# Kernel tuning notes

Hardware: AMD Instinct MI355X
Metric: run time of the kernel (lower is better)

The kernel has to match this reference:

```python
import jax, jax.numpy as jnp
import numpy as np


def _forward(x, wc, we, Wb1, bb1, Wb2, bb2, Wr1, br1, Wr2, br2,
             Wq1, bq1, Wq2, bq2, Wq3, bq3, Wo1, bo1, Wo2, bo2, Wo3, bo3, scale):
    bs, c, h, w = x.shape
    Hs, Ws = scale * h, scale * w
    fh = (jnp.arange(Hs, dtype=jnp.float32) + 0.5) / scale
    fw = (jnp.arange(Ws, dtype=jnp.float32) + 0.5) / scale
    coor_h = fh - jnp.floor(fh + 0.001) - 0.5  # [Hs] fractional phase
    coor_w = fw - jnp.floor(fw + 0.001) - 0.5  # [Ws]
    ones_hw = jnp.ones((Hs, Ws), jnp.float32)
    meta = jnp.stack([ones_hw, ones_hw / scale,
                      jnp.broadcast_to(coor_h[:, None], (Hs, Ws)),
                      jnp.broadcast_to(coor_w[None, :], (Hs, Ws))], 0)  # [4,Hs,Ws]
    chan_mean = x.mean(axis=(0, 2, 3))  # [c]
    chan_scale = jnp.concatenate([chan_mean[:, None], jnp.ones((c, 3), jnp.float32)], axis=1)  # [c,4]
    inp = meta[None] * chan_scale[:, :, None, None]  # [c,4,Hs,Ws]

    # body: 1x1x1 Conv3d over spectral-channel axis c
    lin = lambda W, b, t: jnp.einsum('oc,cfhw->ofhw', W, t) + b[:, None, None, None]
    emb = jax.nn.relu(lin(Wb2, bb2, jax.nn.relu(lin(Wb1, bb1, inp))))  # [c,4,Hs,Ws]

    # offset head: Conv2d 1x1 with batch = c, features = 4 -> 2
    lin2 = lambda W, b, t: jnp.einsum('of,cfhw->cohw', W, t) + b[None, :, None, None]
    off = lin2(Wo3, bo3, jax.nn.relu(lin2(Wo2, bo2, jax.nn.relu(lin2(Wo1, bo1, emb)))))  # [c,2,Hs,Ws]

    # routing_1: Conv3d over c -> 1 channel, sigmoid
    r = jax.nn.sigmoid(lin(Wr2, br2, jax.nn.relu(lin(Wr1, br1, emb))))[0]  # [4,Hs,Ws]
    # routing_2: Conv2d 1x1 over the 4 meta-features -> E experts
    lin3 = lambda W, b, t: jnp.einsum('of,fhw->ohw', W, t) + b[:, None, None]
    rw = jax.nn.sigmoid(lin3(Wq3, bq3, jax.nn.relu(lin3(Wq2, bq2, jax.nn.relu(lin3(Wq1, bq1, r))))))  # [E,Hs,Ws]

    # per-channel offset grid_sample (bilinear, zeros padding, align_corners=True)
    px0 = fw - 0.5  # [Ws] base source x coord
    py0 = fh - 0.5  # [Hs]

    def sample(img, offx, offy):  # img [bs,h,w]; off* [Hs,Ws]
        px = px0[None, :] + offx
        py = py0[:, None] + offy
        x0 = jnp.floor(px); y0 = jnp.floor(py)
        wx = px - x0; wy = py - y0
        x0i = x0.astype(jnp.int32); y0i = y0.astype(jnp.int32)
        def g(yi, xi):
            v = ((xi >= 0) & (xi <= w - 1) & (yi >= 0) & (yi <= h - 1)).astype(img.dtype)
            return img[:, jnp.clip(yi, 0, h - 1), jnp.clip(xi, 0, w - 1)] * v[None]
        return (g(y0i, x0i) * ((1 - wy) * (1 - wx))[None]
                + g(y0i, x0i + 1) * ((1 - wy) * wx)[None]
                + g(y0i + 1, x0i) * (wy * (1 - wx))[None]
                + g(y0i + 1, x0i + 1) * (wy * wx)[None])

    fea0 = jax.vmap(lambda xi, oi: sample(xi, oi[0], oi[1]),
                    in_axes=(1, 0), out_axes=1)(x, off)  # [bs,c,Hs,Ws]

    # per-pixel expert-mixed compress/expand: (sum_e r_e Wc_e) f then (sum_e r_e We_e)
    mid = jnp.einsum('ehw,ekc,bchw->bkhw', rw, wc, fea0)   # [bs,c//8,Hs,Ws]
    out = jnp.einsum('ehw,eck,bkhw->bchw', rw, we, mid)    # [bs,c,Hs,Ws]
    return out + fea0


def setup_inputs() -> dict:
    key = jax.random.key(0)
    ks = jax.random.split(key, 32)
    bs, c, h, w = 4, 64, 64, 64
    E, k = 4, c // 8
    s = 0.05
    d = {
        'x': jax.random.normal(ks[0], (bs, c, h, w), jnp.float32),
        'wc': jax.random.normal(ks[1], (E, k, c), jnp.float32) * s,
        'we': jax.random.normal(ks[2], (E, c, k), jnp.float32) * s,
        'Wb1': jax.random.normal(ks[3], (c, c), jnp.float32) * s,
        'bb1': jax.random.normal(ks[4], (c,), jnp.float32) * s,
        'Wb2': jax.random.normal(ks[5], (c, c), jnp.float32) * s,
        'bb2': jax.random.normal(ks[6], (c,), jnp.float32) * s,
        'Wr1': jax.random.normal(ks[7], (64, c), jnp.float32) * s,
        'br1': jax.random.normal(ks[8], (64,), jnp.float32) * s,
        'Wr2': jax.random.normal(ks[9], (1, 64), jnp.float32) * s,
        'br2': jax.random.normal(ks[10], (1,), jnp.float32) * s,
        'Wq1': jax.random.normal(ks[11], (64, 4), jnp.float32) * s,
        'bq1': jax.random.normal(ks[12], (64,), jnp.float32) * s,
        'Wq2': jax.random.normal(ks[13], (64, 64), jnp.float32) * s,
        'bq2': jax.random.normal(ks[14], (64,), jnp.float32) * s,
        'Wq3': jax.random.normal(ks[15], (E, 64), jnp.float32) * s,
        'bq3': jax.random.normal(ks[16], (E,), jnp.float32) * s,
        'Wo1': jax.random.normal(ks[17], (64, 4), jnp.float32) * s,
        'bo1': jax.random.normal(ks[18], (64,), jnp.float32) * s,
        'Wo2': jax.random.normal(ks[19], (64, 64), jnp.float32) * s,
        'bo2': jax.random.normal(ks[20], (64,), jnp.float32) * s,
        'Wo3': jax.random.normal(ks[21], (2, 64), jnp.float32) * s,
        'bo3': jax.random.normal(ks[22], (2,), jnp.float32) * s,
        'scale': 4,
    }
    return d


def reference(x, wc, we, Wb1, bb1, Wb2, bb2, Wr1, br1, Wr2, br2,
              Wq1, bq1, Wq2, bq2, Wq3, bq3, Wo1, bo1, Wo2, bo2, Wo3, bo3, scale):
    return _forward(x, wc, we, Wb1, bb1, Wb2, bb2, Wr1, br1, Wr2, br2,
                    Wq1, bq1, Wq2, bq2, Wq3, bq3, Wo1, bo1, Wo2, bo2, Wo3, bo3, int(scale))
```

## Files before the change

### kernel.cpp

```cpp
#include <hip/hip_runtime.h>


__device__ __forceinline__ float relu_(float v){ return fmaxf(v, 0.f); }
__device__ __forceinline__ float sigm_(float v){ return 1.f/(1.f + __expf(-v)); }

__global__ void k_mean(const float* __restrict__ x, float* __restrict__ ws) {
  const int ch = blockIdx.x, b = blockIdx.y, t = threadIdx.x;
  const float* xp = x + (size_t)(b*64 + ch)*4096;
  const float4* p4 = reinterpret_cast<const float4*>(xp);
  float4 v0 = p4[t], v1 = p4[t+256], v2 = p4[t+512], v3 = p4[t+768];
  float s = ((v0.x+v0.y)+(v0.z+v0.w)) + ((v1.x+v1.y)+(v1.z+v1.w))
          + ((v2.x+v2.y)+(v2.z+v2.w)) + ((v3.x+v3.y)+(v3.z+v3.w));
  __shared__ float red[256];
  red[t] = s; __syncthreads();
  for (int off = 128; off > 0; off >>= 1) {
    if (t < off) red[t] += red[t + off];
    __syncthreads();
  }
  if (t == 0) ws[b*64 + ch] = red[0];

  float* dst = ws + 21760 + (size_t)(b*64 + ch)*4752;
  if (t < 66) {
    float4* drow = reinterpret_cast<float4*>(dst + t*72);
    const float4 z = make_float4(0.f, 0.f, 0.f, 0.f);
    if (t == 0 || t == 65) {
      #pragma unroll
      for (int q = 0; q < 18; ++q) drow[q] = z;
    } else {
      const float4* srow = reinterpret_cast<const float4*>(xp + (t-1)*64);
      drow[0] = z;
      #pragma unroll
      for (int q = 0; q < 16; ++q) drow[1+q] = srow[q];
      drow[17] = z;
    }
  }
}

__launch_bounds__(256)
__global__ void k_phase(const float* __restrict__ wc, const float* __restrict__ we,
    const float* __restrict__ Wb1, const float* __restrict__ bb1,
    const float* __restrict__ Wb2, const float* __restrict__ bb2,
    const float* __restrict__ Wr1, const float* __restrict__ br1,
    const float* __restrict__ Wr2, const float* __restrict__ br2,
    const float* __restrict__ Wq1, const float* __restrict__ bq1,
    const float* __restrict__ Wq2, const float* __restrict__ bq2,
    const float* __restrict__ Wq3, const float* __restrict__ bq3,
    const float* __restrict__ Wo1, const float* __restrict__ bo1,
    const float* __restrict__ Wo2, const float* __restrict__ bo2,
    const float* __restrict__ Wo3, const float* __restrict__ bo3,
    float* __restrict__ ws)
{
  const int p = blockIdx.x, pi = p >> 2, pj = p & 3;
  const int t = threadIdx.x;
  const float chv = 0.25f*pi - 0.375f, cwv = 0.25f*pj - 0.375f;

  __shared__ float WbL1[64*66];
  __shared__ float WbL2[64*66];
  __shared__ float WrL1[64*66];
  __shared__ float WqL2[64*66];
  __shared__ __align__(16) float Wo2L[4096];
  __shared__ __align__(16) float Wo1L[256];
  __shared__ __align__(16) float wcL[2048];
  __shared__ __align__(16) float weL[2048];
  __shared__ float Wo3L[128];
  __shared__ float Wq1L[256], Wq3L[256];
  __shared__ float Wr2L[64];
  __shared__ float bb1L[64], bb2L[64], br1L[64], bq1L[64], bq2L[64];
  __shared__ float bo1L[64], bo2L[64];

  __shared__ float meanL[64];
  __shared__ __align__(16) float t1L[64][4];
  __shared__ __align__(16) float embL[64][4];
  __shared__ __align__(16) float rpL[64][4];
  __shared__ float r4[4];
  __shared__ float q1L[64], q2L[64];
  __shared__ float rwL[4];
  __shared__ float oxL[64][4], oyL[64][4];
  __shared__ float oxF[64], oyF[64];

  {
    const float* srcs[4] = {Wb1, Wb2, Wr1, Wq2};
    float* dsts[4] = {WbL1, WbL2, WrL1, WqL2};
    for (int m = 0; m < 4; ++m) {
      const float4* W4 = reinterpret_cast<const float4*>(srcs[m]);
      float* WL = dsts[m];
      for (int v = t; v < 1024; v += 256) {
        float4 d = W4[v];
        const int r = v >> 4, c = (v & 15) << 2;
        float* q = &WL[r*66 + c];
        q[0] = d.x; q[1] = d.y; q[2] = d.z; q[3] = d.w;
      }
    }
    for (int v = t; v < 1024; v += 256)
      reinterpret_cast<float4*>(Wo2L)[v] = reinterpret_cast<const float4*>(Wo2)[v];
    for (int v = t; v < 512; v += 256) {
      reinterpret_cast<float4*>(wcL)[v] = reinterpret_cast<const float4*>(wc)[v];
      reinterpret_cast<float4*>(weL)[v] = reinterpret_cast<const float4*>(we)[v];
    }
    if (t < 64) {
      reinterpret_cast<float4*>(Wo1L)[t] = reinterpret_cast<const float4*>(Wo1)[t];
      reinterpret_cast<float4*>(Wq1L)[t] = reinterpret_cast<const float4*>(Wq1)[t];
      reinterpret_cast<float4*>(Wq3L)[t] = reinterpret_cast<const float4*>(Wq3)[t];
      bb1L[t] = bb1[t]; bb2L[t] = bb2[t]; br1L[t] = br1[t];
      bq1L[t] = bq1[t]; bq2L[t] = bq2[t];
      bo1L[t] = bo1[t]; bo2L[t] = bo2[t];
      Wr2L[t] = Wr2[t];
      const float* wsp = ws;
      meanL[t] = (wsp[t] + wsp[64+t] + wsp[128+t] + wsp[192+t]) * (1.f/16384.f);
    }
    if (t >= 64 && t < 192) Wo3L[t-64] = Wo3[t-64];
  }
  __syncthreads();

  if (t < 64) {
    float a0 = 0.f, as = 0.f;
    const float* row = &WbL1[t*66];
    #pragma unroll 8
    for (int c = 0; c < 64; ++c) { float w = row[c]; a0 += w*meanL[c]; as += w; }
    float bb = bb1L[t];
    t1L[t][0] = relu_(a0 + bb);
    t1L[t][1] = relu_(0.25f*as + bb);
    t1L[t][2] = relu_(chv*as + bb);
    t1L[t][3] = relu_(cwv*as + bb);
  }
  __syncthreads();
  if (t < 64) {
    float bb = bb2L[t];
    float e0=bb,e1=bb,e2=bb,e3=bb;
    const float* row = &WbL2[t*66];
    #pragma unroll 8
    for (int c = 0; c < 64; ++c) {
      float w = row[c];
      float4 tv = *reinterpret_cast<const float4*>(&t1L[c][0]);
      e0 += w*tv.x; e1 += w*tv.y; e2 += w*tv.z; e3 += w*tv.w;
    }
    embL[t][0]=relu_(e0); embL[t][1]=relu_(e1); embL[t][2]=relu_(e2); embL[t][3]=relu_(e3);
  }
  __syncthreads();
  if (t < 64) {
    float bb = br1L[t];
    float p0=bb,p1=bb,p2=bb,p3=bb;
    const float* row = &WrL1[t*66];
    #pragma unroll 8
    for (int c = 0; c < 64; ++c) {
      float w = row[c];
      float4 ev = *reinterpret_cast<const float4*>(&embL[c][0]);
      p0 += w*ev.x; p1 += w*ev.y; p2 += w*ev.z; p3 += w*ev.w;
    }
    rpL[t][0]=relu_(p0); rpL[t][1]=relu_(p1); rpL[t][2]=relu_(p2); rpL[t][3]=relu_(p3);
  }
  __syncthreads();
  if (t < 4) {
    float acc = br2[0];
    #pragma unroll 8
    for (int c = 0; c < 64; ++c) acc += Wr2L[c]*rpL[c][t];
    r4[t] = sigm_(acc);
  }
  __syncthreads();
  if (t < 64) {
    float acc = bq1L[t];
    #pragma unroll
    for (int f = 0; f < 4; ++f) acc += Wq1L[t*4+f]*r4[f];
    q1L[t] = relu_(acc);
  }
  __syncthreads();
  if (t < 64) {
    float acc = bq2L[t];
    const float* row = &WqL2[t*66];
    #pragma unroll 8
    for (int c = 0; c < 64; ++c) acc += row[c]*q1L[c];
    q2L[t] = relu_(acc);
  }
  __syncthreads();
  if (t < 4) {
    float acc = bq3[t];
    #pragma unroll 8
    for (int c = 0; c < 64; ++c) acc += Wq3L[t*64+c]*q2L[c];
    rwL[t] = sigm_(acc);
  }
  __syncthreads();

  {
    const int ch = t & 63, q = t >> 6;
    const float4 e = *reinterpret_cast<const float4*>(&embL[ch][0]);
    float v1[64];
    #pragma unroll
    for (int o = 0; o < 64; ++o) {
      float4 w = *reinterpret_cast<const float4*>(&Wo1L[o*4]);
      v1[o] = relu_(w.x*e.x + w.y*e.y + w.z*e.z + w.w*e.w + bo1L[o]);
    }
    float ox = 0.f, oy = 0.f;
    for (int o = q*16; o < q*16+16; ++o) {
      float acc = bo2L[o];
      const float4* row = reinterpret_cast<const float4*>(&Wo2L[o*64]);
      #pragma unroll
      for (int k = 0; k < 16; ++k) {
        float4 w = row[k];
        acc += w.x*v1[4*k+0] + w.y*v1[4*k+1] + w.z*v1[4*k+2] + w.w*v1[4*k+3];
      }
      acc = relu_(acc);
      ox += Wo3L[o]*acc;
      oy += Wo3L[64+o]*acc;
    }
    oxL[ch][q] = ox; oyL[ch][q] = oy;
  }
  __syncthreads();
  if (t < 64) {
    oxF[t] = oxL[t][0]+oxL[t][1]+oxL[t][2]+oxL[t][3] + bo3[0];
    oyF[t] = oyL[t][0]+oyL[t][1]+oyL[t][2]+oyL[t][3] + bo3[1];
  }
  __syncthreads();

  {
    const float r0 = rwL[0], r1 = rwL[1], r2 = rwL[2], r3 = rwL[3];
    for (int idx = t; idx < 1024; idx += 256) {
      const int ch = idx >> 4, k = idx & 15;
      float v;
      if (k < 8) {
        v = r0*wcL[(0*8+k)*64+ch] + r1*wcL[(1*8+k)*64+ch]
          + r2*wcL[(2*8+k)*64+ch] + r3*wcL[(3*8+k)*64+ch];
      } else {
        const int kk = k - 8;
        v = r0*weL[(0*64+ch)*8+kk] + r1*weL[(1*64+ch)*8+kk]
          + r2*weL[(2*64+ch)*8+kk] + r3*weL[(3*64+ch)*8+kk];
      }
      ws[256 + (p*64+ch)*16 + k] = v;
    }
  }

  if (t < 64) {
    const float B = 0.25f*pj - 0.375f + oxF[t];
    const float bxf = floorf(B);
    const float wx = B - bxf;
    const int bx = min(max((int)bxf, -4), 3);
    const float py = 0.25f*pi - 0.375f + oyF[t];
    const float fy = floorf(py);
    const float wy = py - fy;
    const int y0b = min(max((int)fy, -1), 0);
    const float wx0 = 1.f - wx, wx1 = wx;
    const float wy0 = 1.f - wy, wy1 = wy;
    ws[16640 + p*64 + t] = __int_as_float(t*4752 + (y0b+1)*72 + 4 + bx);
    float4 a;
    a.x = wy0*wx0; a.y = wy0*wx1; a.z = wy1*wx0; a.w = wy1*wx1;
    *reinterpret_cast<float4*>(ws + 17664 + (p*64 + t)*4) = a;
  }
}

__launch_bounds__(256, 4)
__global__ void k_main(const float* __restrict__ ws, float* __restrict__ out) {
  const int i = blockIdx.x;
  const int b = blockIdx.y;
  const int w = __builtin_amdgcn_readfirstlane((int)(threadIdx.x >> 6));
  const int l = threadIdx.x & 63;
  const int p = (i & 3)*4 + w;
  const int iqoff = (i >> 2)*72;

  const float* __restrict__ wmxw = ws + 256   + p*1024;
  const float* __restrict__ pbw  = ws + 16640 + p*64;
  const float* __restrict__ paw  = ws + 17664 + p*256;
  const float* __restrict__ xpb  = ws + 21760 + (size_t)b*304128;

  __shared__ float tile[4096];

  float fea[64];
  float m0=0.f,m1=0.f,m2=0.f,m3=0.f,m4=0.f,m5=0.f,m6=0.f,m7=0.f;

  #pragma unroll
  for (int ch = 0; ch < 64; ++ch) {
    const int base = __float_as_int(pbw[ch]) + iqoff;
    const float4 a  = *reinterpret_cast<const float4*>(paw + ch*4);
    const float4 wa = *reinterpret_cast<const float4*>(wmxw + ch*16);
    const float4 wb = *reinterpret_cast<const float4*>(wmxw + ch*16 + 4);
    const float g00 = xpb[base + l],      g01 = xpb[base + l + 1];
    const float g10 = xpb[base + 72 + l], g11 = xpb[base + 73 + l];
    const float fv = g00*a.x + g01*a.y + g10*a.z + g11*a.w;
    fea[ch] = fv;
    m0 += wa.x*fv; m1 += wa.y*fv; m2 += wa.z*fv; m3 += wa.w*fv;
    m4 += wb.x*fv; m5 += wb.y*fv; m6 += wb.z*fv; m7 += wb.w*fv;
  }

  float* __restrict__ ob = out + (size_t)b*4194304 + i*256;
  const int sw = (w & 1) << 4;
  #pragma unroll
  for (int c4 = 0; c4 < 4; ++c4) {
    #pragma unroll
    for (int cc = 0; cc < 16; ++cc) {
      const int ch = c4*16 + cc;
      const float4 wa = *reinterpret_cast<const float4*>(wmxw + ch*16 + 8);
      const float4 wb = *reinterpret_cast<const float4*>(wmxw + ch*16 + 12);
      float acc = fea[ch];
      acc += wa.x*m0 + wa.y*m1 + wa.z*m2 + wa.w*m3;
      acc += wb.x*m4 + wb.y*m5 + wb.z*m6 + wb.w*m7;
      tile[cc*256 + w*64 + (l ^ sw)] = acc;
    }
    __syncthreads();
    #pragma unroll
    for (int cc = 0; cc < 16; ++cc) {
      const int ch = c4*16 + cc;
      const float v = tile[cc*256 + (l&3)*64 + ((w*16 + (l>>2)) ^ ((l&1)<<4))];
      ob[ch*65536 + w*64 + l] = v;
    }
    __syncthreads();
  }
}

extern "C" void kernel_launch(void* const* d_in, const int* in_sizes, int n_in,
                              void* d_out, int out_size, void* d_ws, size_t ws_size,
                              hipStream_t stream) {
  const float* x   = (const float*)d_in[0];
  const float* wc  = (const float*)d_in[1];
  const float* we  = (const float*)d_in[2];
  const float* Wb1 = (const float*)d_in[3];
  const float* bb1 = (const float*)d_in[4];
  const float* Wb2 = (const float*)d_in[5];
  const float* bb2 = (const float*)d_in[6];
  const float* Wr1 = (const float*)d_in[7];
  const float* br1 = (const float*)d_in[8];
  const float* Wr2 = (const float*)d_in[9];
  const float* br2 = (const float*)d_in[10];
  const float* Wq1 = (const float*)d_in[11];
  const float* bq1 = (const float*)d_in[12];
  const float* Wq2 = (const float*)d_in[13];
  const float* bq2 = (const float*)d_in[14];
  const float* Wq3 = (const float*)d_in[15];
  const float* bq3 = (const float*)d_in[16];
  const float* Wo1 = (const float*)d_in[17];
  const float* bo1 = (const float*)d_in[18];
  const float* Wo2 = (const float*)d_in[19];
  const float* bo2 = (const float*)d_in[20];
  const float* Wo3 = (const float*)d_in[21];
  const float* bo3 = (const float*)d_in[22];
  float* ws  = (float*)d_ws;
  float* out = (float*)d_out;

  k_mean<<<dim3(64, 4), 256, 0, stream>>>(x, ws);
  k_phase<<<16, 256, 0, stream>>>(wc, we, Wb1, bb1, Wb2, bb2, Wr1, br1, Wr2, br2,
                                  Wq1, bq1, Wq2, bq2, Wq3, bq3,
                                  Wo1, bo1, Wo2, bo2, Wo3, bo3, ws);
  k_main<<<dim3(256, 4), 256, 0, stream>>>(ws, out);
}
```

Measured before the change: 177.0 us.

## Split channel loop across two wave groups with LDS reduction and XCD-aware block mapping

k_main now runs 512 threads per block. Each half of the block handles 32 of the 64 channels, and the two halves combine their 8 mid accumulators through LDS before the expansion stage. The per-phase workspace layout is reorganised into separate 8-float records for sampling info, the compress weights and the expand weights. Block indices are remapped so that each batch maps onto specific XCDs, which is meant to improve L2 locality. The aim is to halve per-thread serial work and register pressure (fea shrinks from 64 to 32) and to raise parallelism, at the cost of an extra LDS exchange and barrier plus doubled LDS use.

```diff
diff --git a/kernel.cpp b/kernel.cpp
--- a/kernel.cpp
+++ b/kernel.cpp
@@ -19,7 +19,7 @@
   }
   if (t == 0) ws[b*64 + ch] = red[0];
 
-  float* dst = ws + 21760 + (size_t)(b*64 + ch)*4752;
+  float* dst = ws + 24832 + (size_t)(b*64 + ch)*4752;
   if (t < 66) {
     float4* drow = reinterpret_cast<float4*>(dst + t*72);
     const float4 z = make_float4(0.f, 0.f, 0.f, 0.f);
@@ -213,18 +213,14 @@
 
   {
     const float r0 = rwL[0], r1 = rwL[1], r2 = rwL[2], r3 = rwL[3];
-    for (int idx = t; idx < 1024; idx += 256) {
-      const int ch = idx >> 4, k = idx & 15;
-      float v;
-      if (k < 8) {
-        v = r0*wcL[(0*8+k)*64+ch] + r1*wcL[(1*8+k)*64+ch]
-          + r2*wcL[(2*8+k)*64+ch] + r3*wcL[(3*8+k)*64+ch];
-      } else {
-        const int kk = k - 8;
-        v = r0*weL[(0*64+ch)*8+kk] + r1*weL[(1*64+ch)*8+kk]
-          + r2*weL[(2*64+ch)*8+kk] + r3*weL[(3*64+ch)*8+kk];
-      }
-      ws[256 + (p*64+ch)*16 + k] = v;
+    for (int idx = t; idx < 512; idx += 256) {
+      const int ch = idx >> 3, k = idx & 7;
+      ws[8448 + (p*64+ch)*8 + k] =
+          r0*wcL[(0*8+k)*64+ch] + r1*wcL[(1*8+k)*64+ch]
+        + r2*wcL[(2*8+k)*64+ch] + r3*wcL[(3*8+k)*64+ch];
+      ws[16640 + (p*64+ch)*8 + k] =
+          r0*weL[(0*64+ch)*8+k] + r1*weL[(1*64+ch)*8+k]
+        + r2*weL[(2*64+ch)*8+k] + r3*weL[(3*64+ch)*8+k];
     }
   }
 
@@ -239,65 +235,85 @@
     const int y0b = min(max((int)fy, -1), 0);
     const float wx0 = 1.f - wx, wx1 = wx;
     const float wy0 = 1.f - wy, wy1 = wy;
-    ws[16640 + p*64 + t] = __int_as_float(t*4752 + (y0b+1)*72 + 4 + bx);
-    float4 a;
-    a.x = wy0*wx0; a.y = wy0*wx1; a.z = wy1*wx0; a.w = wy1*wx1;
-    *reinterpret_cast<float4*>(ws + 17664 + (p*64 + t)*4) = a;
+    float* r = ws + 256 + (p*64 + t)*8;
+    r[0] = __int_as_float(t*4752 + (y0b+1)*72 + 4 + bx);
+    r[1] = wy0*wx0; r[2] = wy0*wx1; r[3] = wy1*wx0; r[4] = wy1*wx1;
+    r[5] = 0.f; r[6] = 0.f; r[7] = 0.f;
   }
 }
 
-__launch_bounds__(256, 4)
+__launch_bounds__(512, 4)
 __global__ void k_main(const float* __restrict__ ws, float* __restrict__ out) {
-  const int i = blockIdx.x;
-  const int b = blockIdx.y;
-  const int w = __builtin_amdgcn_readfirstlane((int)(threadIdx.x >> 6));
-  const int l = threadIdx.x & 63;
-  const int p = (i & 3)*4 + w;
+  const int bid = blockIdx.x;
+  const int xcd = bid & 7;
+  const int b   = xcd >> 1;
+  const int i   = ((bid >> 3) << 1) | (xcd & 1);
+  const int tw  = (int)(threadIdx.x >> 6);
+  const int w   = __builtin_amdgcn_readfirstlane(tw & 3);
+  const int h   = __builtin_amdgcn_readfirstlane(tw >> 2);
+  const int l   = threadIdx.x & 63;
+  const int p   = (i & 3)*4 + w;
   const int iqoff = (i >> 2)*72;
-
-  const float* __restrict__ wmxw = ws + 256   + p*1024;
-  const float* __restrict__ pbw  = ws + 16640 + p*64;
-  const float* __restrict__ paw  = ws + 17664 + p*256;
-  const float* __restrict__ xpb  = ws + 21760 + (size_t)b*304128;
-
-  __shared__ float tile[4096];
-
-  float fea[64];
+  const int ch0 = h*32;
+
+  const float* __restrict__ recw = ws + 256   + (p*64 + ch0)*8;
+  const float* __restrict__ wcxw = ws + 8448  + (p*64 + ch0)*8;
+  const float* __restrict__ wexw = ws + 16640 + (p*64 + ch0)*8;
+  const float* __restrict__ xpb  = ws + 24832 + (size_t)b*304128;
+
+  __shared__ float tile[2][4096];
+  __shared__ float midL[2][2048];
+
+  float fea[32];
   float m0=0.f,m1=0.f,m2=0.f,m3=0.f,m4=0.f,m5=0.f,m6=0.f,m7=0.f;
 
   #pragma unroll
-  for (int ch = 0; ch < 64; ++ch) {
-    const int base = __float_as_int(pbw[ch]) + iqoff;
-    const float4 a  = *reinterpret_cast<const float4*>(paw + ch*4);
-    const float4 wa = *reinterpret_cast<const float4*>(wmxw + ch*16);
-    const float4 wb = *reinterpret_cast<const float4*>(wmxw + ch*16 + 4);
+  for (int c = 0; c < 32; ++c) {
+    const float4 ra = *reinterpret_cast<const float4*>(recw + c*8);
+    const float a3  = recw[c*8 + 4];
+    const float4 wa = *reinterpret_cast<const float4*>(wcxw + c*8);
+    const float4 wb = *reinterpret_cast<const float4*>(wcxw + c*8 + 4);
+    const int base = __float_as_int(ra.x) + iqoff;
     const float g00 = xpb[base + l],      g01 = xpb[base + l + 1];
     const float g10 = xpb[base + 72 + l], g11 = xpb[base + 73 + l];
-    const float fv = g00*a.x + g01*a.y + g10*a.z + g11*a.w;
-    fea[ch] = fv;
+    const float fv = g00*ra.y + g01*ra.z + g10*ra.w + g11*a3;
+    fea[c] = fv;
     m0 += wa.x*fv; m1 += wa.y*fv; m2 += wa.z*fv; m3 += wa.w*fv;
     m4 += wb.x*fv; m5 += wb.y*fv; m6 += wb.z*fv; m7 += wb.w*fv;
+  }
+
+  {
+    float4* ms = reinterpret_cast<float4*>(&midL[h][(w*64 + l)*8]);
+    ms[0] = make_float4(m0, m1, m2, m3);
+    ms[1] = make_float4(m4, m5, m6, m7);
+  }
+  __syncthreads();
+  {
+    const float4* mo = reinterpret_cast<const float4*>(&midL[1 - h][(w*64 + l)*8]);
+    float4 olo = mo[0], ohi = mo[1];
+    m0 += olo.x; m1 += olo.y; m2 += olo.z; m3 += olo.w;
+    m4 += ohi.x; m5 += ohi.y; m6 += ohi.z; m7 += ohi.w;
   }
 
   float* __restrict__ ob = out + (size_t)b*4194304 + i*256;
   const int sw = (w & 1) << 4;
   #pragma unroll
-  for (int c4 = 0; c4 < 4; ++c4) {
+  for (int c4 = 0; c4 < 2; ++c4) {
     #pragma unroll
     for (int cc = 0; cc < 16; ++cc) {
-      const int ch = c4*16 + cc;
-      const float4 wa = *reinterpret_cast<const float4*>(wmxw + ch*16 + 8);
-      const float4 wb = *reinterpret_cast<const float4*>(wmxw + ch*16 + 12);
-      float acc = fea[ch];
+      const int c = c4*16 + cc;
+      const float4 wa = *reinterpret_cast<const float4*>(wexw + c*8);
+      const float4 wb = *reinterpret_cast<const float4*>(wexw + c*8 + 4);
+      float acc = fea[c];
       acc += wa.x*m0 + wa.y*m1 + wa.z*m2 + wa.w*m3;
       acc += wb.x*m4 + wb.y*m5 + wb.z*m6 + wb.w*m7;
-      tile[cc*256 + w*64 + (l ^ sw)] = acc;
+      tile[h][cc*256 + w*64 + (l ^ sw)] = acc;
     }
     __syncthreads();
     #pragma unroll
     for (int cc = 0; cc < 16; ++cc) {
-      const int ch = c4*16 + cc;
-      const float v = tile[cc*256 + (l&3)*64 + ((w*16 + (l>>2)) ^ ((l&1)<<4))];
+      const int ch = ch0 + c4*16 + cc;
+      const float v = tile[h][cc*256 + (l&3)*64 + ((w*16 + (l>>2)) ^ ((l&1)<<4))];
       ob[ch*65536 + w*64 + l] = v;
     }
     __syncthreads();
@@ -337,5 +353,5 @@
   k_phase<<<16, 256, 0, stream>>>(wc, we, Wb1, bb1, Wb2, bb2, Wr1, br1, Wr2, br2,
                                   Wq1, bq1, Wq2, bq2, Wq3, bq3,
                                   Wo1, bo1, Wo2, bo2, Wo3, bo3, ws);
-  k_main<<<dim3(256, 4), 256, 0, stream>>>(ws, out);
+  k_main<<<1024, 512, 0, stream>>>(ws, out);
 }
```

Result: faster. 169.0 us (-4.5%).
